# Kernel tuning notes

Hardware: AMD Instinct MI355X
Metric: run time of the kernel (lower is better)

## Reference

```python
import jax, jax.numpy as jnp
import numpy as np

B, L, D, OUT, EXP = 4, 4096, 128, 55, 2
D2 = 2 * D

def _ln(x, g, b):
    m = jnp.mean(x, axis=-1, keepdims=True)
    v = jnp.mean((x - m) ** 2, axis=-1, keepdims=True)
    return (x - m) / jnp.sqrt(v + 1e-5) * g + b

def setup_inputs() -> dict:
    key = jax.random.key(0)
    ks = iter(jax.random.split(key, 32))
    w = lambda shape: jax.random.normal(next(ks), shape, jnp.float32) * 0.02
    inp = {
        'x1': jax.random.normal(next(ks), (B, L, D), jnp.float32),
        'x2': jax.random.normal(next(ks), (B, L, D), jnp.float32),
        'ln1_g': jnp.ones((D,)), 'ln1_b': jnp.zeros((D,)),
        'ln2_g': jnp.ones((D,)), 'ln2_b': jnp.zeros((D,)),
        'Wq': w((D, D)), 'bq': jnp.zeros((D,)),
        'Wv1': w((D, D)), 'bv1': jnp.zeros((D,)),
        'Wk': w((D, D)), 'bk': jnp.zeros((D,)),
        'Wv2': w((D, D)), 'bv2': jnp.zeros((D,)),
        'Wp1': w((D, D)), 'bp1': jnp.zeros((D,)),
        'Wp2': w((D, D)), 'bp2': jnp.zeros((D,)),
        'lnf_g': jnp.ones((D2,)), 'lnf_b': jnp.zeros((D2,)),
        'Wf1': w((D2, EXP * D2)), 'bf1': jnp.zeros((EXP * D2,)),
        'Wf2': w((EXP * D2, D2)), 'bf2': jnp.zeros((D2,)),
        'ln3_g': jnp.ones((D2,)), 'ln3_b': jnp.zeros((D2,)),
        'Wo': w((D2, OUT)), 'bo': jnp.zeros((OUT,)),
    }
    return inp

def reference(x1, x2, ln1_g, ln1_b, ln2_g, ln2_b, Wq, bq, Wv1, bv1, Wk, bk,
              Wv2, bv2, Wp1, bp1, Wp2, bp2, lnf_g, lnf_b, Wf1, bf1, Wf2, bf2,
              ln3_g, ln3_b, Wo, bo):
    res1, res2 = x1, x2
    x1n = _ln(x1, ln1_g, ln1_b)
    x2n = _ln(x2, ln2_g, ln2_b)
    q1 = x1n @ Wq + bq        # [B,L,D]
    v1 = x1n @ Wv1 + bv1
    k2 = x2n @ Wk + bk
    v2 = x2n @ Wv2 + bv2
    # faithful to torch: energy = einsum('bqd,bkd->bqk', keys2, queries1)
    energy = jnp.einsum('bqd,bkd->bqk', k2, q1)
    att = jax.nn.softmax(energy / jnp.sqrt(jnp.float32(D)), axis=-1)  # [B,L,L]
    out1 = jnp.einsum('bal,blv->bav', att, v1) @ Wp1 + bp1
    out2 = jnp.einsum('bal,blv->bav', att, v2) @ Wp2 + bp2
    y1 = out1 + res1
    y2 = out2 + res2
    x = jnp.concatenate([y1, y2], axis=-1)  # [B,L,2D]
    res = x
    h = _ln(x, lnf_g, lnf_b)
    h = jax.nn.gelu(h @ Wf1 + bf1, approximate=False) @ Wf2 + bf2
    x = _ln(h + res, ln3_g, ln3_b)
    return x @ Wo + bo  # [B,L,OUT]
```

## Files before the change

kernel.cpp:

```cpp
#include <hip/hip_runtime.h>
#include <hip/hip_fp16.h>

typedef _Float16 half8 __attribute__((ext_vector_type(8)));
typedef float f32x4 __attribute__((ext_vector_type(4)));
typedef long lng2 __attribute__((ext_vector_type(2)));

#define B_   4
#define L_   4096
#define D_   128
#define M_   (B_*L_)
#define D2_  256
#define H_   512
#define OUT_ 55

__device__ __forceinline__ f32x4 mfma16(half8 a, half8 b, f32x4 c) {
    return __builtin_amdgcn_mfma_f32_16x16x32_f16(a, b, c, 0, 0, 0);
}
__device__ __forceinline__ f32x4 mfma8(long a, long b, f32x4 c) {
    return __builtin_amdgcn_mfma_f32_16x16x32_fp8_fp8(a, b, c, 0, 0, 0);
}
__device__ __forceinline__ int pk4(float a, float b, float c, float d) {
    int t = __builtin_amdgcn_cvt_pk_fp8_f32(a, b, 0, false);
    return __builtin_amdgcn_cvt_pk_fp8_f32(c, d, t, true);
}

#define KSCL (0.08838834764831845f * 1.4426950408889634f)

#define WQ_OFF   0
#define WV1_OFF  16384
#define WK_OFF   32768
#define WV2_OFF  49152
#define WP1_OFF  65536
#define WP2_OFF  81920
#define WF1_OFF  98304
#define WF2_OFF  229376
#define WO_OFF   360448


__global__ void prep_kernel(const float* Wq, const float* Wv1, const float* Wk,
                            const float* Wv2, const float* Wp1, const float* Wp2,
                            const float* Wf1, const float* Wf2, const float* Wo,
                            _Float16* wsw) {
    int id = blockIdx.y;
    int t  = blockIdx.x * 256 + threadIdx.x;
    const float* src = nullptr; int K = 0, N = 0, Npad = 0, off = 0;
    switch (id) {
        case 0: src = Wq;  K = 128; N = 128; Npad = 128; off = WQ_OFF;  break;
        case 1: src = Wv1; K = 128; N = 128; Npad = 128; off = WV1_OFF; break;
        case 2: src = Wk;  K = 128; N = 128; Npad = 128; off = WK_OFF;  break;
        case 3: src = Wv2; K = 128; N = 128; Npad = 128; off = WV2_OFF; break;
        case 4: src = Wp1; K = 128; N = 128; Npad = 128; off = WP1_OFF; break;
        case 5: src = Wp2; K = 128; N = 128; Npad = 128; off = WP2_OFF; break;
        case 6: src = Wf1; K = 256; N = 512; Npad = 512; off = WF1_OFF; break;
        case 7: src = Wf2; K = 512; N = 256; Npad = 256; off = WF2_OFF; break;
        case 8: src = Wo;  K = 256; N = 55;  Npad = 64;  off = WO_OFF;  break;
        default: return;
    }
    int total = K * Npad;
    if (t >= total) return;
    int k = t / Npad, n = t % Npad;
    float v = (n < N) ? src[k * N + n] : 0.f;
    int s = k >> 5, c = n >> 4, ln = n & 15;
    int q, j;
    if (id == 4 || id == 5) { q = (k >> 2) & 3; j = (k & 3) + (((k >> 4) & 1) << 2); }
    else                    { q = (k >> 3) & 3; j = k & 7; }
    int nc = Npad >> 4;
    wsw[off + ((size_t)((s * nc + c) * 64 + q * 16 + ln)) * 8 + j] = (_Float16)v;
}


__global__ __launch_bounds__(256) void ln_kernel(const float* x1, const float* x2,
        const float* g1, const float* b1, const float* g2, const float* b2,
        _Float16* x1n, _Float16* x2n) {
    int wave = threadIdx.x >> 6, lane = threadIdx.x & 63;
    int token = blockIdx.x * 4 + wave;
    const float* x = blockIdx.y ? x2 : x1;
    const float* g = blockIdx.y ? g2 : g1;
    const float* bb = blockIdx.y ? b2 : b1;
    _Float16* o = blockIdx.y ? x2n : x1n;
    const float* xr = x + (size_t)token * D_;
    float a0 = xr[lane], a1 = xr[lane + 64];
    float s = a0 + a1, s2 = a0 * a0 + a1 * a1;
    #pragma unroll
    for (int off = 1; off < 64; off <<= 1) {
        s += __shfl_xor(s, off);
        s2 += __shfl_xor(s2, off);
    }
    float mean = s * (1.f / 128.f);
    float var = s2 * (1.f / 128.f) - mean * mean;
    float inv = rsqrtf(var + 1e-5f);
    int lt = token >> 4, ln_r = token & 15;
    #pragma unroll
    for (int h = 0; h < 2; h++) {
        int col = lane + h * 64;
        float v = (h ? a1 : a0);
        float out = (v - mean) * inv * g[col] + bb[col];
        int ss = col >> 5, q = (col >> 3) & 3, j = col & 7;
        o[((size_t)((lt * 4 + ss) * 64 + q * 16 + ln_r)) * 8 + j] = (_Float16)out;
    }
}

__global__ __launch_bounds__(256) void proj_kernel(const _Float16* x1n, const _Float16* x2n,
        const _Float16* wsw, const float* bq, const float* bv1, const float* bk,
        const float* bv2, _Float16* q1, _Float16* k2, unsigned char* vsw8) {
    int g = blockIdx.y;
    const _Float16* A = (g < 2) ? x1n : x2n;
    const _Float16* Bw = wsw + g * 16384;
    const float* bias = (g == 0) ? bq : (g == 1) ? bv1 : (g == 2) ? bk : bv2;
    int wave = threadIdx.x >> 6, lane = threadIdx.x & 63;
    int quad = lane >> 4, ln = lane & 15;
    int mbase = blockIdx.x * 64 + wave * 16;
    int lt = mbase >> 4;

    half8 a[4];
    #pragma unroll
    for (int s = 0; s < 4; s++)
        a[s] = *(const half8*)(A + ((size_t)((lt * 4 + s) * 64 + lane)) * 8);

    f32x4 acc[8];
    #pragma unroll
    for (int c = 0; c < 8; c++) {
        acc[c] = f32x4{0.f, 0.f, 0.f, 0.f};
        #pragma unroll
        for (int s = 0; s < 4; s++) {
            half8 bf = *(const half8*)(Bw + ((size_t)((s * 8 + c) * 64 + lane)) * 8);
            acc[c] = mfma16(a[s], bf, acc[c]);
        }
    }
    bool isV = (g == 1) || (g == 3);
    if (!isV) {
        float scl = (g == 2) ? KSCL : 1.f;
        _Float16* out = (g == 0) ? q1 : k2;
        #pragma unroll
        for (int c = 0; c < 8; c++) {
            int n = c * 16 + ln;
            float bv = bias[n];
            #pragma unroll
            for (int r = 0; r < 4; r++) {
                int s_o = c >> 1, q_o = ((c & 1) << 1) | (ln >> 3), j = ln & 7;
                out[((size_t)((lt * 4 + s_o) * 64 + q_o * 16 + (quad * 4 + r))) * 8 + j]
                    = (_Float16)((acc[c][r] + bv) * scl);
            }
        }
    } else {
        int cbase = (g == 3) ? 8 : 0;
        int b = mbase >> 12;
        int l0 = (mbase & (L_ - 1)) + quad * 4;
        int sp = l0 >> 6, tt = (l0 >> 4) & 3, q2 = (l0 >> 2) & 3;
        unsigned char* Vb = vsw8 + (size_t)b * (1u << 20);
        #pragma unroll
        for (int c = 0; c < 8; c++) {
            int n = c * 16 + ln;
            float bv = bias[n];
            int pk = pk4(acc[c][0] + bv, acc[c][1] + bv, acc[c][2] + bv, acc[c][3] + bv);
            *(int*)(Vb + (((size_t)(sp * 16 + cbase + c) * 64 + q2 * 16 + ln) * 16 + tt * 4)) = pk;
        }
    }
}

__global__ __launch_bounds__(256) void zero_kernel(float* rowsum) {
    int i = (blockIdx.x * 256 + threadIdx.x) * 4;
    *(f32x4*)(rowsum + i) = f32x4{0.f, 0.f, 0.f, 0.f};
}

__global__ __launch_bounds__(256) void score_kernel(
        const _Float16* __restrict__ q1sw, const _Float16* __restrict__ k2sw,
        unsigned char* __restrict__ pmat8, float* __restrict__ rowsum) {
    int w = threadIdx.x >> 6, lane = threadIdx.x & 63;
    int quad = lane >> 4, ln = lane & 15;
    int b = blockIdx.z;
    int kL0 = blockIdx.y * 128 + (w & 1) * 64;
    int mL0 = blockIdx.x * 128 + (w >> 1) * 64;
    int ltk = ((b << 12) + kL0) >> 4;
    int ltm = ((b << 12) + mL0) >> 4;

    f32x4 acc[4][4];
    #pragma unroll
    for (int i = 0; i < 4; i++)
        #pragma unroll
        for (int j = 0; j < 4; j++) acc[i][j] = f32x4{0.f, 0.f, 0.f, 0.f};

    #pragma unroll
    for (int s = 0; s < 4; s++) {
        half8 a[4], bq[4];
        #pragma unroll
        for (int i = 0; i < 4; i++)
            a[i] = *(const half8*)(q1sw + ((size_t)(((ltk + i) * 4 + s) * 64 + lane)) * 8);
        #pragma unroll
        for (int j = 0; j < 4; j++)
            bq[j] = *(const half8*)(k2sw + ((size_t)(((ltm + j) * 4 + s) * 64 + lane)) * 8);
        #pragma unroll
        for (int i = 0; i < 4; i++)
            #pragma unroll
            for (int j = 0; j < 4; j++)
                acc[i][j] = mfma16(a[i], bq[j], acc[i][j]);
    }

    unsigned char* Pb = pmat8 + (size_t)b * (16u << 20);
    int sp = kL0 >> 6;
    #pragma unroll
    for (int j = 0; j < 4; j++) {
        int4 d;
        float csum = 0.f;
        #pragma unroll
        for (int i = 0; i < 4; i++) {
            float p0 = exp2f(acc[i][j][0]);
            float p1 = exp2f(acc[i][j][1]);
            float p2 = exp2f(acc[i][j][2]);
            float p3 = exp2f(acc[i][j][3]);
            csum += (p0 + p1) + (p2 + p3);
            ((int*)&d)[i] = pk4(p0, p1, p2, p3);
        }
        csum += __shfl_xor(csum, 16);
        csum += __shfl_xor(csum, 32);
        if (lane < 16)
            atomicAdd(&rowsum[(b << 12) + mL0 + j * 16 + ln], csum);
        int lt = (mL0 >> 4) + j;
        *(int4*)(Pb + (((size_t)(lt * 64 + sp)) * 64 + lane) * 16) = d;
    }
}

__global__ __launch_bounds__(256) void pv_kernel(
        const unsigned char* __restrict__ pmat8, const unsigned char* __restrict__ vsw8,
        const float* __restrict__ rowsum,
        _Float16* __restrict__ att1, _Float16* __restrict__ att2) {
    int w = threadIdx.x >> 6, lane = threadIdx.x & 63;
    int quad = lane >> 4, ln = lane & 15;
    int rowG0 = blockIdx.x * 32;
    int b = rowG0 >> 12;
    int lt0 = (rowG0 & (L_ - 1)) >> 4;
    const unsigned char* Pb = pmat8 + (size_t)b * (16u << 20);
    const unsigned char* Vb = vsw8 + (size_t)b * (1u << 20);

    f32x4 acc[4][2];
    #pragma unroll
    for (int i = 0; i < 4; i++)
        #pragma unroll
        for (int c = 0; c < 2; c++) acc[i][c] = f32x4{0.f, 0.f, 0.f, 0.f};

    lng2 Vf[2][4], Pf[2][2];
    #pragma unroll
    for (int p = 0; p < 2; p++) {
        #pragma unroll
        for (int i = 0; i < 4; i++)
            Vf[p][i] = *(const lng2*)(Vb + (((size_t)(p * 16 + w * 4 + i)) * 64 + lane) * 16);
        #pragma unroll
        for (int c = 0; c < 2; c++)
            Pf[p][c] = *(const lng2*)(Pb + (((size_t)((lt0 + c) * 64 + p)) * 64 + lane) * 16);
    }

    #define PVSTEP(buf, sp) do {                                                     \
        int spn = ((sp) + 2 < 64) ? (sp) + 2 : 63;                                   \
        lng2 Vn[4], Pn[2];                                                           \
        _Pragma("unroll")                                                            \
        for (int i = 0; i < 4; i++)                                                  \
            Vn[i] = *(const lng2*)(Vb + (((size_t)(spn * 16 + w * 4 + i)) * 64 + lane) * 16); \
        _Pragma("unroll")                                                            \
        for (int c = 0; c < 2; c++)                                                  \
            Pn[c] = *(const lng2*)(Pb + (((size_t)((lt0 + c) * 64 + spn)) * 64 + lane) * 16); \
        _Pragma("unroll")                                                            \
        for (int i = 0; i < 4; i++)                                                  \
            _Pragma("unroll")                                                        \
            for (int c = 0; c < 2; c++) {                                            \
                acc[i][c] = mfma8(Vf[buf][i].x, Pf[buf][c].x, acc[i][c]);             \
                acc[i][c] = mfma8(Vf[buf][i].y, Pf[buf][c].y, acc[i][c]);             \
            }                                                                        \
        _Pragma("unroll")                                                            \
        for (int i = 0; i < 4; i++) Vf[buf][i] = Vn[i];                              \
        _Pragma("unroll")                                                            \
        for (int c = 0; c < 2; c++) Pf[buf][c] = Pn[c];                              \
    } while (0)

    for (int sp = 0; sp < 64; sp += 2) {
        PVSTEP(0, sp);
        PVSTEP(1, sp + 1);
    }
    #undef PVSTEP

    _Float16* att = (w >= 2) ? att2 : att1;
    #pragma unroll
    for (int c = 0; c < 2; c++) {
        float inv = 1.f / rowsum[rowG0 + c * 16 + ln];
        int lt = (rowG0 >> 4) + c;
        #pragma unroll
        for (int sl = 0; sl < 2; sl++) {
            half8 v;
            #pragma unroll
            for (int r = 0; r < 4; r++) {
                v[r]     = (_Float16)(acc[2 * sl][c][r] * inv);
                v[r + 4] = (_Float16)(acc[2 * sl + 1][c][r] * inv);
            }
            int s = (w & 1) * 2 + sl;
            *(half8*)(att + ((size_t)((lt * 4 + s) * 64 + lane)) * 8) = v;
        }
    }
}

__global__ __launch_bounds__(256) void attn_out_kernel(const _Float16* att1, const _Float16* att2,
        const _Float16* wsw, const float* bp1, const float* bp2,
        const float* x1, const float* x2, const float* lnf_g, const float* lnf_b,
        _Float16* res, _Float16* xn) {
    int wave = threadIdx.x >> 6, lane = threadIdx.x & 63;
    int quad = lane >> 4, ln = lane & 15;
    int mbase = blockIdx.x * 64 + wave * 16;
    int lt = mbase >> 4;
    const _Float16* Wp1 = wsw + WP1_OFF;
    const _Float16* Wp2 = wsw + WP2_OFF;

    half8 a1[4], a2[4];
    #pragma unroll
    for (int s = 0; s < 4; s++) {
        a1[s] = *(const half8*)(att1 + ((size_t)((lt * 4 + s) * 64 + lane)) * 8);
        a2[s] = *(const half8*)(att2 + ((size_t)((lt * 4 + s) * 64 + lane)) * 8);
    }
    f32x4 y1[8], y2[8];
    #pragma unroll
    for (int c = 0; c < 8; c++) {
        y1[c] = f32x4{0,0,0,0}; y2[c] = f32x4{0,0,0,0};
        #pragma unroll
        for (int s = 0; s < 4; s++) {
            y1[c] = mfma16(a1[s], *(const half8*)(Wp1 + ((size_t)((s * 8 + c) * 64 + lane)) * 8), y1[c]);
            y2[c] = mfma16(a2[s], *(const half8*)(Wp2 + ((size_t)((s * 8 + c) * 64 + lane)) * 8), y2[c]);
        }
    }
    #pragma unroll
    for (int c = 0; c < 8; c++) {
        int n = c * 16 + ln;
        float b1v = bp1[n], b2v = bp2[n];
        #pragma unroll
        for (int r = 0; r < 4; r++) {
            int m = mbase + quad * 4 + r;
            y1[c][r] += b1v + x1[(size_t)m * D_ + n];
            y2[c][r] += b2v + x2[(size_t)m * D_ + n];
        }
    }
    float sum[4] = {0,0,0,0}, sq[4] = {0,0,0,0};
    #pragma unroll
    for (int c = 0; c < 8; c++)
        #pragma unroll
        for (int r = 0; r < 4; r++) {
            sum[r] += y1[c][r] + y2[c][r];
            sq[r]  += y1[c][r] * y1[c][r] + y2[c][r] * y2[c][r];
        }
    #pragma unroll
    for (int off = 1; off < 16; off <<= 1)
        #pragma unroll
        for (int r = 0; r < 4; r++) { sum[r] += __shfl_xor(sum[r], off); sq[r] += __shfl_xor(sq[r], off); }
    #pragma unroll
    for (int r = 0; r < 4; r++) {
        float mean = sum[r] * (1.f / 256.f);
        float var = sq[r] * (1.f / 256.f) - mean * mean;
        float inv = rsqrtf(var + 1e-5f);
        int m = mbase + quad * 4 + r;
        int lt_m = m >> 4;
        #pragma unroll
        for (int c = 0; c < 8; c++) {
            int n = c * 16 + ln;
            res[(size_t)m * D2_ + n]       = (_Float16)y1[c][r];
            res[(size_t)m * D2_ + 128 + n] = (_Float16)y2[c][r];
            float yn1 = (y1[c][r] - mean) * inv * lnf_g[n] + lnf_b[n];
            float yn2 = (y2[c][r] - mean) * inv * lnf_g[128 + n] + lnf_b[128 + n];
            int s_x = n >> 5, q_x = (n >> 3) & 3, j = n & 7;
            xn[((size_t)((lt_m * 8 + s_x) * 64 + q_x * 16 + (m & 15))) * 8 + j] = (_Float16)yn1;
            int n2 = 128 + n;
            int s_y = n2 >> 5, q_y = (n2 >> 3) & 3, j2 = n2 & 7;
            xn[((size_t)((lt_m * 8 + s_y) * 64 + q_y * 16 + (m & 15))) * 8 + j2] = (_Float16)yn2;
        }
    }
}

__global__ __launch_bounds__(256) void ffn1_kernel(const _Float16* xn, const _Float16* wsw,
        const float* bf1, _Float16* h) {
    int wave = threadIdx.x >> 6, lane = threadIdx.x & 63;
    int quad = lane >> 4, ln = lane & 15;
    int mbase = blockIdx.x * 64 + wave * 16;
    int lt = mbase >> 4;
    int nt = blockIdx.y;
    const _Float16* W = wsw + WF1_OFF;

    half8 a[8];
    #pragma unroll
    for (int s = 0; s < 8; s++)
        a[s] = *(const half8*)(xn + ((size_t)((lt * 8 + s) * 64 + lane)) * 8);

    f32x4 acc[8];
    #pragma unroll
    for (int c = 0; c < 8; c++) acc[c] = f32x4{0,0,0,0};

    half8 Wc[8], Wn[8];
    #pragma unroll
    for (int s = 0; s < 8; s++)
        Wc[s] = *(const half8*)(W + ((size_t)((s * 32 + nt * 8) * 64 + lane)) * 8);
    #pragma unroll
    for (int c = 0; c < 8; c++) {
        int cn = (c < 7) ? c + 1 : 7;
        #pragma unroll
        for (int s = 0; s < 8; s++)
            Wn[s] = *(const half8*)(W + ((size_t)((s * 32 + nt * 8 + cn) * 64 + lane)) * 8);
        #pragma unroll
        for (int s = 0; s < 8; s++)
            acc[c] = mfma16(a[s], Wc[s], acc[c]);
        #pragma unroll
        for (int s = 0; s < 8; s++) Wc[s] = Wn[s];
    }
    #pragma unroll
    for (int c = 0; c < 8; c++) {
        int n = nt * 128 + c * 16 + ln;
        float bv = bf1[n];
        int s_h = n >> 5, q_h = (n >> 3) & 3, j = n & 7;
        #pragma unroll
        for (int r = 0; r < 4; r++) {
            float v = acc[c][r] + bv;
            float ge = 0.5f * v * (1.f + erff(v * 0.70710678118654752f));
            h[((size_t)((lt * 16 + s_h) * 64 + q_h * 16 + (quad * 4 + r))) * 8 + j] = (_Float16)ge;
        }
    }
}

__global__ __launch_bounds__(256) void ffn2_kernel(const _Float16* h, const _Float16* wsw,
        const float* bf2, const _Float16* res, const float* g3, const float* b3, _Float16* xn2) {
    __shared__ float sst[2][16][2][2];
    int w = threadIdx.x >> 6, lane = threadIdx.x & 63;
    int quad = lane >> 4, ln = lane & 15;
    int rt = w & 1, nh = w >> 1;
    int mb = blockIdx.x * 32 + rt * 16;
    int lt = mb >> 4;
    const _Float16* W = wsw + WF2_OFF;

    f32x4 acc[8];
    #pragma unroll
    for (int c = 0; c < 8; c++) acc[c] = f32x4{0,0,0,0};

    half8 aC, aN;
    half8 Wc[8], Wn[8];
    aC = *(const half8*)(h + ((size_t)((lt * 16 + 0) * 64 + lane)) * 8);
    #pragma unroll
    for (int c = 0; c < 8; c++)
        Wc[c] = *(const half8*)(W + ((size_t)((0 * 16 + nh * 8 + c) * 64 + lane)) * 8);

    #pragma unroll
    for (int s = 0; s < 16; s++) {
        int sn = (s < 15) ? s + 1 : 15;
        aN = *(const half8*)(h + ((size_t)((lt * 16 + sn) * 64 + lane)) * 8);
        #pragma unroll
        for (int c = 0; c < 8; c++)
            Wn[c] = *(const half8*)(W + ((size_t)((sn * 16 + nh * 8 + c) * 64 + lane)) * 8);
        #pragma unroll
        for (int c = 0; c < 8; c++)
            acc[c] = mfma16(aC, Wc[c], acc[c]);
        aC = aN;
        #pragma unroll
        for (int c = 0; c < 8; c++) Wc[c] = Wn[c];
    }

    float y[8][4];
    float psum[4] = {0,0,0,0}, psq[4] = {0,0,0,0};
    #pragma unroll
    for (int c = 0; c < 8; c++) {
        int n = nh * 128 + c * 16 + ln;
        float bv = bf2[n];
        #pragma unroll
        for (int r = 0; r < 4; r++) {
            int m = mb + quad * 4 + r;
            float v = acc[c][r] + bv + (float)res[(size_t)m * D2_ + n];
            y[c][r] = v; psum[r] += v; psq[r] += v * v;
        }
    }
    #pragma unroll
    for (int off = 1; off < 16; off <<= 1)
        #pragma unroll
        for (int r = 0; r < 4; r++) { psum[r] += __shfl_xor(psum[r], off); psq[r] += __shfl_xor(psq[r], off); }
    if (ln == 0)
        #pragma unroll
        for (int r = 0; r < 4; r++) { sst[rt][quad * 4 + r][nh][0] = psum[r]; sst[rt][quad * 4 + r][nh][1] = psq[r]; }
    __syncthreads();
    #pragma unroll
    for (int r = 0; r < 4; r++) {
        float su = sst[rt][quad * 4 + r][0][0] + sst[rt][quad * 4 + r][1][0];
        float sq = sst[rt][quad * 4 + r][0][1] + sst[rt][quad * 4 + r][1][1];
        float mean = su * (1.f / 256.f);
        float var = sq * (1.f / 256.f) - mean * mean;
        float invs = rsqrtf(var + 1e-5f);
        #pragma unroll
        for (int c = 0; c < 8; c++) {
            int n = nh * 128 + c * 16 + ln;
            float yn = (y[c][r] - mean) * invs * g3[n] + b3[n];
            int s_x = n >> 5, q_x = (n >> 3) & 3, j = n & 7;
            xn2[((size_t)((lt * 8 + s_x) * 64 + q_x * 16 + (quad * 4 + r))) * 8 + j] = (_Float16)yn;
        }
    }
}

__global__ __launch_bounds__(256) void out_kernel(const _Float16* xn2, const _Float16* wsw,
        const float* bo, float* out) {
    __shared__ f32x4 pc[2][4][64];
    int w = threadIdx.x >> 6, lane = threadIdx.x & 63;
    int quad = lane >> 4, ln = lane & 15;
    int rt = w & 1, kh = w >> 1;
    int mb = blockIdx.x * 32 + rt * 16;
    int lt = mb >> 4;
    const _Float16* W = wsw + WO_OFF;

    f32x4 acc[4];
    #pragma unroll
    for (int c = 0; c < 4; c++) acc[c] = f32x4{0,0,0,0};
    #pragma unroll
    for (int ss = 0; ss < 4; ss++) {
        int s = kh * 4 + ss;
        half8 a = *(const half8*)(xn2 + ((size_t)((lt * 8 + s) * 64 + lane)) * 8);
        #pragma unroll
        for (int c = 0; c < 4; c++)
            acc[c] = mfma16(a, *(const half8*)(W + ((size_t)((s * 4 + c) * 64 + lane)) * 8), acc[c]);
    }
    if (kh == 1)
        #pragma unroll
        for (int c = 0; c < 4; c++) pc[rt][c][lane] = acc[c];
    __syncthreads();
    if (kh == 0) {
        #pragma unroll
        for (int c = 0; c < 4; c++) {
            f32x4 p = pc[rt][c][lane];
            int n = c * 16 + ln;
            if (n < OUT_) {
                float bv = bo[n];
                #pragma unroll
                for (int r = 0; r < 4; r++)
                    out[(size_t)(mb + quad * 4 + r) * OUT_ + n] = acc[c][r] + p[r] + bv;
            }
        }
    }
}

extern "C" void kernel_launch(void* const* d_in, const int* in_sizes, int n_in,
                              void* d_out, int out_size, void* d_ws, size_t ws_size,
                              hipStream_t stream) {
    const float* x1    = (const float*)d_in[0];
    const float* x2    = (const float*)d_in[1];
    const float* ln1_g = (const float*)d_in[2];
    const float* ln1_b = (const float*)d_in[3];
    const float* ln2_g = (const float*)d_in[4];
    const float* ln2_b = (const float*)d_in[5];
    const float* Wq    = (const float*)d_in[6];
    const float* bq    = (const float*)d_in[7];
    const float* Wv1   = (const float*)d_in[8];
    const float* bv1   = (const float*)d_in[9];
    const float* Wk    = (const float*)d_in[10];
    const float* bk    = (const float*)d_in[11];
    const float* Wv2   = (const float*)d_in[12];
    const float* bv2   = (const float*)d_in[13];
    const float* Wp1   = (const float*)d_in[14];
    const float* bp1   = (const float*)d_in[15];
    const float* Wp2   = (const float*)d_in[16];
    const float* bp2   = (const float*)d_in[17];
    const float* lnf_g = (const float*)d_in[18];
    const float* lnf_b = (const float*)d_in[19];
    const float* Wf1   = (const float*)d_in[20];
    const float* bf1   = (const float*)d_in[21];
    const float* Wf2   = (const float*)d_in[22];
    const float* bf2   = (const float*)d_in[23];
    const float* ln3_g = (const float*)d_in[24];
    const float* ln3_b = (const float*)d_in[25];
    const float* Wo    = (const float*)d_in[26];
    const float* bo    = (const float*)d_in[27];
    float* out = (float*)d_out;

    char* ws = (char*)d_ws;
    const size_t MB = 1 << 20;
    _Float16* q1sw   = (_Float16*)(ws + 0 * MB);
    _Float16* k2sw   = (_Float16*)(ws + 4 * MB);
    unsigned char* vsw8 = (unsigned char*)(ws + 8 * MB);
    _Float16* att1   = (_Float16*)(ws + 12 * MB);
    _Float16* att2   = (_Float16*)(ws + 16 * MB);
    _Float16* x1n    = (_Float16*)(ws + 20 * MB);
    _Float16* x2n    = (_Float16*)(ws + 24 * MB);
    _Float16* wsw    = (_Float16*)(ws + 28 * MB);
    float*    rowsum = (float*)   (ws + 29 * MB);
    _Float16* res    = (_Float16*)(ws + 30 * MB);
    _Float16* xn     = (_Float16*)(ws + 46 * MB);
    _Float16* h      = (_Float16*)(ws + 54 * MB);
    _Float16* xn2    = (_Float16*)(ws + 70 * MB);
    unsigned char* pmat8 = (unsigned char*)(ws + 78 * MB);

    prep_kernel<<<dim3(512, 9), 256, 0, stream>>>(Wq, Wv1, Wk, Wv2, Wp1, Wp2, Wf1, Wf2, Wo, wsw);
    ln_kernel<<<dim3(M_ / 4, 2), 256, 0, stream>>>(x1, x2, ln1_g, ln1_b, ln2_g, ln2_b, x1n, x2n);
    proj_kernel<<<dim3(M_ / 64, 4), 256, 0, stream>>>(x1n, x2n, wsw, bq, bv1, bk, bv2,
                                                      q1sw, k2sw, vsw8);
    zero_kernel<<<dim3(16), 256, 0, stream>>>(rowsum);
    score_kernel<<<dim3(32, 32, 4), 256, 0, stream>>>(q1sw, k2sw, pmat8, rowsum);
    pv_kernel<<<dim3(M_ / 32), 256, 0, stream>>>(pmat8, vsw8, rowsum, att1, att2);
    attn_out_kernel<<<dim3(M_ / 64), 256, 0, stream>>>(att1, att2, wsw, bp1, bp2,
                                                       x1, x2, lnf_g, lnf_b, res, xn);
    ffn1_kernel<<<dim3(M_ / 64, 4), 256, 0, stream>>>(xn, wsw, bf1, h);
    ffn2_kernel<<<dim3(M_ / 32), 256, 0, stream>>>(h, wsw, bf2, res, ln3_g, ln3_b, xn2);
    out_kernel<<<dim3(M_ / 32), 256, 0, stream>>>(xn2, wsw, bo, out);
}
```

Before: 257.6 us.

## Prefetch weight fragments in projection GEMMs, use fast exp2 and tanh-approx GELU

Software-prefetches the next column's weight fragments in the QKV and output-projection kernels so global loads overlap the MFMAs. Replaces exp2f with the raw hardware exp2 intrinsic in the attention-score kernel. Replaces exact erf GELU with a tanh-approximate GELU computed via hardware exp2 and reciprocal, which changes the numerics slightly. These target load latency and transcendental instruction cost, at the price of extra registers and a small accuracy deviation from the exact-GELU reference.

```diff
diff --git a/kernel.cpp b/kernel.cpp
--- a/kernel.cpp
+++ b/kernel.cpp
@@ -23,6 +23,7 @@
     int t = __builtin_amdgcn_cvt_pk_fp8_f32(a, b, 0, false);
     return __builtin_amdgcn_cvt_pk_fp8_f32(c, d, t, true);
 }
+__device__ __forceinline__ float fexp2(float x) { return __builtin_amdgcn_exp2f(x); }
 
 #define KSCL (0.08838834764831845f * 1.4426950408889634f)
 
@@ -119,14 +120,25 @@
 
     f32x4 acc[8];
     #pragma unroll
+    for (int c = 0; c < 8; c++) acc[c] = f32x4{0.f, 0.f, 0.f, 0.f};
+
+    half8 Wc[4], Wn[4];
+    #pragma unroll
+    for (int s = 0; s < 4; s++)
+        Wc[s] = *(const half8*)(Bw + ((size_t)((s * 8 + 0) * 64 + lane)) * 8);
+    #pragma unroll
     for (int c = 0; c < 8; c++) {
-        acc[c] = f32x4{0.f, 0.f, 0.f, 0.f};
-        #pragma unroll
-        for (int s = 0; s < 4; s++) {
-            half8 bf = *(const half8*)(Bw + ((size_t)((s * 8 + c) * 64 + lane)) * 8);
-            acc[c] = mfma16(a[s], bf, acc[c]);
-        }
-    }
+        int cn = (c < 7) ? c + 1 : 7;
+        #pragma unroll
+        for (int s = 0; s < 4; s++)
+            Wn[s] = *(const half8*)(Bw + ((size_t)((s * 8 + cn) * 64 + lane)) * 8);
+        #pragma unroll
+        for (int s = 0; s < 4; s++)
+            acc[c] = mfma16(a[s], Wc[s], acc[c]);
+        #pragma unroll
+        for (int s = 0; s < 4; s++) Wc[s] = Wn[s];
+    }
+
     bool isV = (g == 1) || (g == 3);
     if (!isV) {
         float scl = (g == 2) ? KSCL : 1.f;
@@ -204,10 +216,10 @@
         float csum = 0.f;
         #pragma unroll
         for (int i = 0; i < 4; i++) {
-            float p0 = exp2f(acc[i][j][0]);
-            float p1 = exp2f(acc[i][j][1]);
-            float p2 = exp2f(acc[i][j][2]);
-            float p3 = exp2f(acc[i][j][3]);
+            float p0 = fexp2(acc[i][j][0]);
+            float p1 = fexp2(acc[i][j][1]);
+            float p2 = fexp2(acc[i][j][2]);
+            float p3 = fexp2(acc[i][j][3]);
             csum += (p0 + p1) + (p2 + p3);
             ((int*)&d)[i] = pk4(p0, p1, p2, p3);
         }
@@ -315,14 +327,31 @@
     }
     f32x4 y1[8], y2[8];
     #pragma unroll
+    for (int c = 0; c < 8; c++) { y1[c] = f32x4{0,0,0,0}; y2[c] = f32x4{0,0,0,0}; }
+
+    half8 W1c[4], W2c[4], W1n[4], W2n[4];
+    #pragma unroll
+    for (int s = 0; s < 4; s++) {
+        W1c[s] = *(const half8*)(Wp1 + ((size_t)((s * 8 + 0) * 64 + lane)) * 8);
+        W2c[s] = *(const half8*)(Wp2 + ((size_t)((s * 8 + 0) * 64 + lane)) * 8);
+    }
+    #pragma unroll
     for (int c = 0; c < 8; c++) {
-        y1[c] = f32x4{0,0,0,0}; y2[c] = f32x4{0,0,0,0};
+        int cn = (c < 7) ? c + 1 : 7;
         #pragma unroll
         for (int s = 0; s < 4; s++) {
-            y1[c] = mfma16(a1[s], *(const half8*)(Wp1 + ((size_t)((s * 8 + c) * 64 + lane)) * 8), y1[c]);
-            y2[c] = mfma16(a2[s], *(const half8*)(Wp2 + ((size_t)((s * 8 + c) * 64 + lane)) * 8), y2[c]);
-        }
-    }
+            W1n[s] = *(const half8*)(Wp1 + ((size_t)((s * 8 + cn) * 64 + lane)) * 8);
+            W2n[s] = *(const half8*)(Wp2 + ((size_t)((s * 8 + cn) * 64 + lane)) * 8);
+        }
+        #pragma unroll
+        for (int s = 0; s < 4; s++) {
+            y1[c] = mfma16(a1[s], W1c[s], y1[c]);
+            y2[c] = mfma16(a2[s], W2c[s], y2[c]);
+        }
+        #pragma unroll
+        for (int s = 0; s < 4; s++) { W1c[s] = W1n[s]; W2c[s] = W2n[s]; }
+    }
+
     #pragma unroll
     for (int c = 0; c < 8; c++) {
         int n = c * 16 + ln;
@@ -411,7 +440,9 @@
         #pragma unroll
         for (int r = 0; r < 4; r++) {
             float v = acc[c][r] + bv;
-            float ge = 0.5f * v * (1.f + erff(v * 0.70710678118654752f));
+            float u = 0.7978845608f * (v + 0.044715f * v * v * v);
+            float e = fexp2(-2.8853900818f * u);
+            float ge = v * __builtin_amdgcn_rcpf(1.f + e);
             h[((size_t)((lt * 16 + s_h) * 64 + q_h * 16 + (quad * 4 + r))) * 8 + j] = (_Float16)ge;
         }
     }
```

Measured after the change: 249.6 us. 1.03x faster.
